# Performance work log

Hardware: AMD Instinct MI355X
Metric: run time of the kernel (lower is better)

## Reference

```python
import jax, jax.numpy as jnp
import numpy as np

B, C, N, H = 8, 256, 1024, 8

def setup_inputs() -> dict:
    key = jax.random.key(0)
    ks = jax.random.split(key, 6)
    x = jax.random.normal(ks[0], (B, C, 3, N), jnp.float32)
    scale = 1.0 / np.sqrt(C).astype(np.float32)
    Wq = jax.random.normal(ks[1], (C, C), jnp.float32) * scale
    Wk = jax.random.normal(ks[2], (C, C), jnp.float32) * scale
    Wv = jax.random.normal(ks[3], (C, C), jnp.float32) * scale
    Wp = jax.random.normal(ks[4], (C, C), jnp.float32) * scale
    mask = jax.random.randint(ks[5], (B, N), 0, 2).astype(bool)  # True = padded
    return {"x": x, "Wq": Wq, "Wk": Wk, "Wv": Wv, "Wp": Wp, "mask": mask}

def _vn_linear(W, x):
    # VNLinear: channel-mixing linear (no bias) over the C axis of [B, C, 3, N]
    return jnp.einsum('oc,bcdn->bodn', W, x)

def _to_heads(t):
    # [B, C, 3, N] -> [B, H, N, (C//H)*3]
    hd = C // H
    return t.reshape(B, H, hd, 3, N).transpose(0, 1, 4, 2, 3).reshape(B, H, N, hd * 3)

def reference(x, Wq, Wk, Wv, Wp, mask):
    hd = C // H
    D = hd * 3
    q = _to_heads(_vn_linear(Wq, x))
    k = _to_heads(_vn_linear(Wk, x))
    v = _to_heads(_vn_linear(Wv, x))
    att = jnp.einsum('bhnd,bhmd->bhnm', q, k) * (1.0 / np.sqrt(D).astype(np.float32))
    att = jnp.where(mask[:, None, None, :], -jnp.inf, att)
    att = jax.nn.softmax(att, axis=-1)
    y = jnp.einsum('bhnm,bhmd->bhnd', att, v)
    # [B, H, N, D] -> [B, H, D, N] -> [B, H, hd, 3, N] -> [B, C, 3, N]
    y = y.transpose(0, 1, 3, 2).reshape(B, H, hd, 3, N).reshape(B, C, 3, N)
    return _vn_linear(Wp, y)
```

## Files before the change

### kernel.cpp

```cpp
#include <hip/hip_runtime.h>
#include <hip/hip_bf16.h>
#include <math.h>

#define B_ 8
#define C_ 256
#define N_ 1024
#define H_ 8
#define DH 96
#define BHN (C_*3*N_)
#define SC 0.10206207261596575f

typedef _Float16 half8 __attribute__((ext_vector_type(8)));
typedef float f32x4 __attribute__((ext_vector_type(4)));
typedef float f32x16 __attribute__((ext_vector_type(16)));

typedef __attribute__((address_space(1))) void gvoid;
typedef __attribute__((address_space(3))) void lvoid;
__device__ inline void gl_lds16(const _Float16* g, _Float16* l) {
  __builtin_amdgcn_global_load_lds((gvoid*)g, (lvoid*)l, 16, 0, 0);
}

typedef __fp16 fp16x2 __attribute__((ext_vector_type(2)));
union H2U { fp16x2 h2; unsigned u; };
__device__ inline unsigned pkh(float a, float b) {
  H2U x; x.h2 = __builtin_amdgcn_cvt_pkrtz(a, b); return x.u;
}
union PF { half8 v; unsigned u[4]; };

__global__ void mask_bits_kernel(const unsigned* __restrict__ mraw,
                                 unsigned long long* __restrict__ mb) {
  __shared__ int notI, notF;
  if (threadIdx.x == 0) { notI = 0; notF = 0; }
  __syncthreads();
  int li = 0, lf = 0;
  for (int i = threadIdx.x; i < 2048; i += 256) {
    unsigned w = mraw[i];
    if (w > 1u) li = 1;
    if (w != 0u && w != 0x3F800000u) lf = 1;
  }
  if (li) atomicOr(&notI, 1);
  if (lf) atomicOr(&notF, 1);
  __syncthreads();
  const int tid = threadIdx.x;
  if (tid < 128) {
    int base = tid * 64;
    unsigned long long bits = 0;
    if (!notI) {
      for (int j = 0; j < 64; ++j)
        bits |= (unsigned long long)(mraw[base + j] & 1u) << j;
    } else if (!notF) {
      for (int j = 0; j < 64; ++j)
        bits |= (unsigned long long)(mraw[base + j] != 0u ? 1 : 0) << j;
    } else {
      const unsigned char* m8 = (const unsigned char*)mraw;
      for (int j = 0; j < 64; ++j)
        bits |= (unsigned long long)(m8[base + j] ? 1 : 0) << j;
    }
    mb[tid] = bits;
  }
}

__global__ void convw_kernel(const float* __restrict__ Wq,
                             const float* __restrict__ Wk,
                             const float* __restrict__ Wv,
                             const float* __restrict__ Wp,
                             _Float16* __restrict__ Wh) {
  int idx = blockIdx.x * 256 + threadIdx.x;
  int e0 = idx * 8;
  const float* src = (e0 < 65536) ? Wq
                   : (e0 < 131072) ? Wk
                   : (e0 < 196608) ? Wv : Wp;
  int off = e0 & 65535;
  float4 a = *(const float4*)&src[off];
  float4 b = *(const float4*)&src[off + 4];
  _Float16 t[8] = {(_Float16)a.x, (_Float16)a.y, (_Float16)a.z, (_Float16)a.w,
                   (_Float16)b.x, (_Float16)b.y, (_Float16)b.z, (_Float16)b.w};
  *(uint4*)&Wh[e0] = *(uint4*)t;
}

__global__ __launch_bounds__(256) void convxt_kernel(
    const float* __restrict__ x, _Float16* __restrict__ XT) {
  __shared__ _Float16 T[64][65];
  const int m0 = blockIdx.x * 64;
  const int c0 = blockIdx.y * 64;
  const int b = blockIdx.z;
  const float* xb = x + (size_t)b * BHN;
  _Float16* ob = XT + (size_t)b * BHN;
  const int t = threadIdx.x;
#pragma unroll
  for (int i = 0; i < 16; ++i) {
    int e = t + i * 256;
    int c = e >> 6, m = e & 63;
    T[m][c] = (_Float16)xb[(size_t)(c0 + c) * 3072 + m0 + m];
  }
  __syncthreads();
#pragma unroll
  for (int i = 0; i < 2; ++i) {
    int e = t + i * 256;
    int m = e >> 3, ch = e & 7;
    _Float16 tmp[8];
#pragma unroll
    for (int j = 0; j < 8; ++j) tmp[j] = T[m][ch * 8 + j];
    *(uint4*)&ob[(size_t)(m0 + m) * 256 + c0 + ch * 8] = *(uint4*)tmp;
  }
}

template <int MODE>
__global__ __launch_bounds__(256, 4) void mgemm_kernel(
    const _Float16* __restrict__ Wh, int woff,
    const _Float16* __restrict__ Xn,
    _Float16* __restrict__ O0, _Float16* __restrict__ O1,
    _Float16* __restrict__ O2, float* __restrict__ Of, int nw) {
  const int zz = blockIdx.z;
  const int w = zz % nw;
  const int b = zz / nw;
  const _Float16* Wb = Wh + (size_t)(woff + w) * 65536;
  const _Float16* Bb = Xn + (size_t)b * BHN;
  const int o0 = blockIdx.y * 128;
  const int bn0 = blockIdx.x * 128;

  __shared__ __align__(16) _Float16 Ah[4096];
  __shared__ __align__(16) _Float16 Bh[4096];

  const int tid = threadIdx.x;
  const int wave = tid >> 6;
  const int lane = tid & 63;
  const int lg = lane >> 4, ll = lane & 15;
  const int wm = wave >> 1, wn = wave & 1;
  const int r0 = tid >> 2, c4 = tid & 3;

  f32x4 acc[4][4];
#pragma unroll
  for (int mi = 0; mi < 4; ++mi)
#pragma unroll
    for (int ni = 0; ni < 4; ++ni) acc[mi][ni] = (f32x4){0.f, 0.f, 0.f, 0.f};

  for (int k0 = 0; k0 < 256; k0 += 32) {
    gl_lds16(Wb + (size_t)(o0 + r0) * 256 + k0 + c4 * 8, &Ah[wave * 512]);
    gl_lds16(Wb + (size_t)(o0 + 64 + r0) * 256 + k0 + c4 * 8,
             &Ah[2048 + wave * 512]);
    gl_lds16(Bb + (size_t)(bn0 + r0) * 256 + k0 + c4 * 8, &Bh[wave * 512]);
    gl_lds16(Bb + (size_t)(bn0 + 64 + r0) * 256 + k0 + c4 * 8,
             &Bh[2048 + wave * 512]);
    __syncthreads();
    half8 af[4], bf[4];
#pragma unroll
    for (int mi = 0; mi < 4; ++mi)
      af[mi] = *(const half8*)&Ah[(wm * 64 + mi * 16 + ll) * 32 + lg * 8];
#pragma unroll
    for (int ni = 0; ni < 4; ++ni)
      bf[ni] = *(const half8*)&Bh[(wn * 64 + ni * 16 + ll) * 32 + lg * 8];
#pragma unroll
    for (int mi = 0; mi < 4; ++mi)
#pragma unroll
      for (int ni = 0; ni < 4; ++ni)
        acc[mi][ni] = __builtin_amdgcn_mfma_f32_16x16x32_f16(
            af[mi], bf[ni], acc[mi][ni], 0, 0, 0);
    __syncthreads();
  }

#pragma unroll
  for (int mi = 0; mi < 4; ++mi) {
#pragma unroll
    for (int ni = 0; ni < 4; ++ni) {
      int o = o0 + wm * 64 + mi * 16 + lg * 4;
      int n = bn0 + wn * 64 + ni * 16 + ll;
      if constexpr (MODE == 1) {
        float* Ofb = Of + (size_t)b * BHN;
#pragma unroll
        for (int r = 0; r < 4; ++r)
          Ofb[(size_t)(o + r) * 3072 + n] = acc[mi][ni][r];
      } else {
        if (w == 2) {
          _Float16* Oc = O2 + (size_t)b * BHN;
#pragma unroll
          for (int r = 0; r < 4; ++r)
            Oc[(size_t)(o + r) * 3072 + n] = (_Float16)acc[mi][ni][r];
        } else {
          _Float16* On = ((w == 0) ? O0 : O1) + (size_t)b * BHN;
          float qs = (w == 0) ? SC : 1.0f;
          _Float16 t4[4];
#pragma unroll
          for (int r = 0; r < 4; ++r) t4[r] = (_Float16)(acc[mi][ni][r] * qs);
          *(uint2*)&On[(size_t)n * 256 + o] = *(uint2*)t4;
        }
      }
    }
  }
}

__global__ __launch_bounds__(256, 2) void attn_kernel(
    const _Float16* __restrict__ qh, const _Float16* __restrict__ kh,
    const _Float16* __restrict__ vh,
    const unsigned long long* __restrict__ mbits,
    _Float16* __restrict__ yT) {
  const int gid = blockIdx.x;
  const int bh = gid & 63;
  const int qt = gid >> 6;
  const int b = bh >> 3, h = bh & 7;
  const int n0 = qt * 128;

  __shared__ __align__(16) _Float16 Qs[12288];
  __shared__ __align__(16) _Float16 Ks[6144];
  __shared__ __align__(16) _Float16 Vt[6144];

  const int tid = threadIdx.x;
  const int lane = tid & 63;
  const int wave = tid >> 6;
  const int hi = lane >> 5;
  const int lq = lane & 31;
  const int wq0 = wave * 32;

  const _Float16* qb = qh + (size_t)b * BHN;
  const _Float16* kb = kh + (size_t)b * BHN;
  const _Float16* vb = vh + (size_t)b * BHN;

#pragma unroll
  for (int r = 0; r < 6; ++r) {
    int pc = r * 4 + wave;
    int p = pc >> 1;
    int q = (pc & 1) * 64 + lane;
    gl_lds16(qb + (size_t)((p >> 2) * 1024 + n0 + q) * 256 + h * 32 + (p & 3) * 8,
             &Qs[(r * 4 + wave) * 512]);
  }
  __syncthreads();

  half8 qf[6];
#pragma unroll
  for (int ks = 0; ks < 6; ++ks)
    qf[ks] = *(const half8*)&Qs[(((2 * ks + hi) * 128) + wq0 + lq) * 8];

  const _Float16* ksrc[3];
  const _Float16* vsrc[3];
#pragma unroll
  for (int r = 0; r < 3; ++r) {
    int p = r * 4 + wave;
    ksrc[r] = kb + (size_t)((p >> 2) * 1024 + lane) * 256 + h * 32 + (p & 3) * 8;
    int G = (r * 4 + wave) * 64 + lane;
    int kp = G / 96, d = G - kp * 96;
    vsrc[r] = vb + (size_t)(h * 32 + (d & 31)) * 3072 + (d >> 5) * 1024 + kp * 8;
  }

  float M = 0.f, L = 0.f;
  f32x16 yacc[3];
#pragma unroll
  for (int dt = 0; dt < 3; ++dt)
#pragma unroll
    for (int r = 0; r < 16; ++r) yacc[dt][r] = 0.f;

  for (int t = 0; t < 16; ++t) {
    __syncthreads();
#pragma unroll
    for (int r = 0; r < 3; ++r) {
      gl_lds16(ksrc[r], &Ks[(r * 4 + wave) * 512]);
      gl_lds16(vsrc[r], &Vt[(r * 4 + wave) * 512]);
      ksrc[r] += 64 * 256;
      vsrc[r] += 64;
    }
    __syncthreads();

    const unsigned long long m64 = mbits[b * 16 + t];

    f32x16 s[2];
#pragma unroll
    for (int r = 0; r < 16; ++r) { s[0][r] = 0.f; s[1][r] = 0.f; }
#pragma unroll
    for (int ks = 0; ks < 6; ++ks) {
      half8 kf0 = *(const half8*)&Ks[(((2 * ks + hi) * 64) + lq) * 8];
      half8 kf1 = *(const half8*)&Ks[(((2 * ks + hi) * 64) + 32 + lq) * 8];
      s[0] = __builtin_amdgcn_mfma_f32_32x32x16_f16(kf0, qf[ks], s[0], 0, 0, 0);
      s[1] = __builtin_amdgcn_mfma_f32_32x32x16_f16(kf1, qf[ks], s[1], 0, 0, 0);
    }

    float mx = -1e30f;
#pragma unroll
    for (int nt = 0; nt < 2; ++nt) {
      unsigned wm = (unsigned)(m64 >> (nt * 32 + 4 * hi));
#pragma unroll
      for (int r = 0; r < 16; ++r) {
        float sv = s[nt][r];
        sv = ((wm >> ((r & 3) + 8 * (r >> 2))) & 1u) ? -1e30f : sv;
        s[nt][r] = sv;
        mx = fmaxf(mx, sv);
      }
    }
    mx = fmaxf(mx, __shfl_xor(mx, 32));
    float newM = fmaxf(M, mx);
    float corr = __expf(M - newM);
    M = newM;
    float psum = 0.f;
#pragma unroll
    for (int nt = 0; nt < 2; ++nt)
#pragma unroll
      for (int r = 0; r < 16; ++r) {
        float p = __expf(s[nt][r] - newM);
        s[nt][r] = p;
        psum += p;
      }
    psum += __shfl_xor(psum, 32);
    L = L * corr + psum;
#pragma unroll
    for (int dt = 0; dt < 3; ++dt)
#pragma unroll
      for (int r = 0; r < 16; ++r) yacc[dt][r] *= corr;

#pragma unroll
    for (int nt = 0; nt < 2; ++nt) {
#pragma unroll
      for (int hf = 0; hf < 2; ++hf) {
        const int bs = hf * 8;
        unsigned A0 = pkh(s[nt][bs + 0], s[nt][bs + 1]);
        unsigned A1 = pkh(s[nt][bs + 2], s[nt][bs + 3]);
        unsigned B0 = pkh(s[nt][bs + 4], s[nt][bs + 5]);
        unsigned B1 = pkh(s[nt][bs + 6], s[nt][bs + 7]);
        unsigned xA0 = (unsigned)__shfl_xor((int)A0, 32);
        unsigned xA1 = (unsigned)__shfl_xor((int)A1, 32);
        unsigned xB0 = (unsigned)__shfl_xor((int)B0, 32);
        unsigned xB1 = (unsigned)__shfl_xor((int)B1, 32);
        PF pf;
        pf.u[0] = hi ? xB0 : A0;
        pf.u[1] = hi ? xB1 : A1;
        pf.u[2] = hi ? B0 : xA0;
        pf.u[3] = hi ? B1 : xA1;
        const int kt = nt * 2 + hf;
#pragma unroll
        for (int dt = 0; dt < 3; ++dt) {
          half8 vf = *(const half8*)&Vt[(((kt * 2 + hi) * 96) + dt * 32 + lq) * 8];
          yacc[dt] = __builtin_amdgcn_mfma_f32_32x32x16_f16(vf, pf.v, yacc[dt],
                                                            0, 0, 0);
        }
      }
    }
  }

  float inv = (L > 0.f) ? 1.f / L : 0.f;
  _Float16* Ys = &Qs[wave * 3072];
#pragma unroll
  for (int dt = 0; dt < 3; ++dt)
#pragma unroll
    for (int r = 0; r < 16; ++r) {
      int dperm = dt * 32 + (r & 3) + 8 * (r >> 2) + 4 * hi;
      Ys[lq * 96 + dperm] = (_Float16)(yacc[dt][r] * inv);
    }
  _Float16* yb = yT + (size_t)b * BHN;
#pragma unroll
  for (int j = 0; j < 6; ++j) {
    int c = j * 64 + lane;
    int q = c / 12, p = c - q * 12;
    uint4 val = *(const uint4*)&Ys[q * 96 + p * 8];
    int dd = p >> 2, pi = p & 3;
    *(uint4*)&yb[(size_t)((dd << 10) + n0 + wq0 + q) * 256 + h * 32 + pi * 8] =
        val;
  }
}

extern "C" void kernel_launch(void* const* d_in, const int* in_sizes, int n_in,
                              void* d_out, int out_size, void* d_ws,
                              size_t ws_size, hipStream_t stream) {
  const float* x = (const float*)d_in[0];
  const float* Wq = (const float*)d_in[1];
  const float* Wk = (const float*)d_in[2];
  const float* Wv = (const float*)d_in[3];
  const float* Wp = (const float*)d_in[4];
  const unsigned* mask = (const unsigned*)d_in[5];
  float* out = (float*)d_out;

  _Float16* Wh = (_Float16*)d_ws;
  _Float16* XT = Wh + 4 * 65536;
  _Float16* qh = XT + (size_t)B_ * BHN;
  _Float16* kh = qh + (size_t)B_ * BHN;
  _Float16* vh = kh + (size_t)B_ * BHN;
  _Float16* yT = vh + (size_t)B_ * BHN;
  unsigned long long* mb = (unsigned long long*)(yT + (size_t)B_ * BHN);

  mask_bits_kernel<<<1, 256, 0, stream>>>(mask, mb);
  convw_kernel<<<128, 256, 0, stream>>>(Wq, Wk, Wv, Wp, Wh);
  convxt_kernel<<<dim3(48, 4, B_), 256, 0, stream>>>(x, XT);

  dim3 g1(24, 2, B_ * 3);
  mgemm_kernel<0><<<g1, 256, 0, stream>>>(Wh, 0, XT, qh, kh, vh, nullptr, 3);

  attn_kernel<<<dim3(512), 256, 0, stream>>>(qh, kh, vh, mb, yT);

  dim3 g3(24, 2, B_);
  mgemm_kernel<1><<<g3, 256, 0, stream>>>(Wh, 3, yT, nullptr, nullptr, nullptr,
                                          out, 1);
}
```

Before: 104.9 us.

## Double-buffer K/V tiles, add lazy softmax rescaling and permlane32 swaps

K and V tiles now go into two LDS buffers, so the async global-to-LDS load of tile t+1 is issued while tile t is computed. This removes one barrier per iteration and hides load latency. The online softmax only rescales the accumulators when some row max grows by more than 8, and the row-sum shuffle is deferred to the end. The four xor-32 shuffles that build the P operand are replaced by two v_permlane32_swap instructions, and MFMA sections are wrapped in s_setprio. The extra LDS buffer raises shared memory per block, which could limit occupancy, and the lazy rescale lets fp16 P values grow up to about e^8.

```diff
diff --git a/kernel.cpp b/kernel.cpp
--- a/kernel.cpp
+++ b/kernel.cpp
@@ -26,6 +26,10 @@
   H2U x; x.h2 = __builtin_amdgcn_cvt_pkrtz(a, b); return x.u;
 }
 union PF { half8 v; unsigned u[4]; };
+
+__device__ inline void plswap(unsigned& a, unsigned& b) {
+  asm volatile("v_permlane32_swap_b32 %0, %1" : "+v"(a), "+v"(b));
+}
 
 __global__ void mask_bits_kernel(const unsigned* __restrict__ mraw,
                                  unsigned long long* __restrict__ mb) {
@@ -201,8 +205,8 @@
   const int n0 = qt * 128;
 
   __shared__ __align__(16) _Float16 Qs[12288];
-  __shared__ __align__(16) _Float16 Ks[6144];
-  __shared__ __align__(16) _Float16 Vt[6144];
+  __shared__ __align__(16) _Float16 KsL[2][6144];
+  __shared__ __align__(16) _Float16 VtL[2][6144];
 
   const int tid = threadIdx.x;
   const int lane = tid & 63;
@@ -215,6 +219,29 @@
   const _Float16* kb = kh + (size_t)b * BHN;
   const _Float16* vb = vh + (size_t)b * BHN;
 
+  const _Float16* ksrc[3];
+  const _Float16* vsrc[3];
+#pragma unroll
+  for (int r = 0; r < 3; ++r) {
+    int p = r * 4 + wave;
+    ksrc[r] = kb + (size_t)((p >> 2) * 1024 + lane) * 256 + h * 32 + (p & 3) * 8;
+    int G = (r * 4 + wave) * 64 + lane;
+    int kp = G / 96, d = G - kp * 96;
+    vsrc[r] = vb + (size_t)(h * 32 + (d & 31)) * 3072 + (d >> 5) * 1024 + kp * 8;
+  }
+
+  auto stage_kv = [&](int cur) {
+    _Float16* Kd = &KsL[cur][0];
+    _Float16* Vd = &VtL[cur][0];
+#pragma unroll
+    for (int r = 0; r < 3; ++r) {
+      gl_lds16(ksrc[r], &Kd[(r * 4 + wave) * 512]);
+      gl_lds16(vsrc[r], &Vd[(r * 4 + wave) * 512]);
+      ksrc[r] += 64 * 256;
+      vsrc[r] += 64;
+    }
+  };
+
 #pragma unroll
   for (int r = 0; r < 6; ++r) {
     int pc = r * 4 + wave;
@@ -223,54 +250,39 @@
     gl_lds16(qb + (size_t)((p >> 2) * 1024 + n0 + q) * 256 + h * 32 + (p & 3) * 8,
              &Qs[(r * 4 + wave) * 512]);
   }
+  stage_kv(0);
   __syncthreads();
+  stage_kv(1);
 
   half8 qf[6];
 #pragma unroll
   for (int ks = 0; ks < 6; ++ks)
     qf[ks] = *(const half8*)&Qs[(((2 * ks + hi) * 128) + wq0 + lq) * 8];
 
-  const _Float16* ksrc[3];
-  const _Float16* vsrc[3];
-#pragma unroll
-  for (int r = 0; r < 3; ++r) {
-    int p = r * 4 + wave;
-    ksrc[r] = kb + (size_t)((p >> 2) * 1024 + lane) * 256 + h * 32 + (p & 3) * 8;
-    int G = (r * 4 + wave) * 64 + lane;
-    int kp = G / 96, d = G - kp * 96;
-    vsrc[r] = vb + (size_t)(h * 32 + (d & 31)) * 3072 + (d >> 5) * 1024 + kp * 8;
-  }
-
-  float M = 0.f, L = 0.f;
+  float M = 0.f, Lh = 0.f;
   f32x16 yacc[3];
 #pragma unroll
   for (int dt = 0; dt < 3; ++dt)
 #pragma unroll
     for (int r = 0; r < 16; ++r) yacc[dt][r] = 0.f;
 
-  for (int t = 0; t < 16; ++t) {
-    __syncthreads();
-#pragma unroll
-    for (int r = 0; r < 3; ++r) {
-      gl_lds16(ksrc[r], &Ks[(r * 4 + wave) * 512]);
-      gl_lds16(vsrc[r], &Vt[(r * 4 + wave) * 512]);
-      ksrc[r] += 64 * 256;
-      vsrc[r] += 64;
-    }
-    __syncthreads();
-
+  auto compute_tile = [&](int t, int cur) {
+    const _Float16* Ksb = &KsL[cur][0];
+    const _Float16* Vtb = &VtL[cur][0];
     const unsigned long long m64 = mbits[b * 16 + t];
 
     f32x16 s[2];
 #pragma unroll
     for (int r = 0; r < 16; ++r) { s[0][r] = 0.f; s[1][r] = 0.f; }
+    __builtin_amdgcn_s_setprio(1);
 #pragma unroll
     for (int ks = 0; ks < 6; ++ks) {
-      half8 kf0 = *(const half8*)&Ks[(((2 * ks + hi) * 64) + lq) * 8];
-      half8 kf1 = *(const half8*)&Ks[(((2 * ks + hi) * 64) + 32 + lq) * 8];
+      half8 kf0 = *(const half8*)&Ksb[(((2 * ks + hi) * 64) + lq) * 8];
+      half8 kf1 = *(const half8*)&Ksb[(((2 * ks + hi) * 64) + 32 + lq) * 8];
       s[0] = __builtin_amdgcn_mfma_f32_32x32x16_f16(kf0, qf[ks], s[0], 0, 0, 0);
       s[1] = __builtin_amdgcn_mfma_f32_32x32x16_f16(kf1, qf[ks], s[1], 0, 0, 0);
     }
+    __builtin_amdgcn_s_setprio(0);
 
     float mx = -1e30f;
 #pragma unroll
@@ -284,25 +296,27 @@
         mx = fmaxf(mx, sv);
       }
     }
-    mx = fmaxf(mx, __shfl_xor(mx, 32));
-    float newM = fmaxf(M, mx);
-    float corr = __expf(M - newM);
-    M = newM;
+    if (__any(mx > M + 8.f)) {
+      float mx2 = fmaxf(mx, __shfl_xor(mx, 32));
+      float newM = fmaxf(M, mx2);
+      float corr = __expf(M - newM);
+      M = newM;
+      Lh *= corr;
+#pragma unroll
+      for (int dt = 0; dt < 3; ++dt)
+#pragma unroll
+        for (int r = 0; r < 16; ++r) yacc[dt][r] *= corr;
+    }
     float psum = 0.f;
 #pragma unroll
     for (int nt = 0; nt < 2; ++nt)
 #pragma unroll
       for (int r = 0; r < 16; ++r) {
-        float p = __expf(s[nt][r] - newM);
+        float p = __expf(s[nt][r] - M);
         s[nt][r] = p;
         psum += p;
       }
-    psum += __shfl_xor(psum, 32);
-    L = L * corr + psum;
-#pragma unroll
-    for (int dt = 0; dt < 3; ++dt)
-#pragma unroll
-      for (int r = 0; r < 16; ++r) yacc[dt][r] *= corr;
+    Lh += psum;
 
 #pragma unroll
     for (int nt = 0; nt < 2; ++nt) {
@@ -313,26 +327,34 @@
         unsigned A1 = pkh(s[nt][bs + 2], s[nt][bs + 3]);
         unsigned B0 = pkh(s[nt][bs + 4], s[nt][bs + 5]);
         unsigned B1 = pkh(s[nt][bs + 6], s[nt][bs + 7]);
-        unsigned xA0 = (unsigned)__shfl_xor((int)A0, 32);
-        unsigned xA1 = (unsigned)__shfl_xor((int)A1, 32);
-        unsigned xB0 = (unsigned)__shfl_xor((int)B0, 32);
-        unsigned xB1 = (unsigned)__shfl_xor((int)B1, 32);
+        plswap(A0, B0);
+        plswap(A1, B1);
         PF pf;
-        pf.u[0] = hi ? xB0 : A0;
-        pf.u[1] = hi ? xB1 : A1;
-        pf.u[2] = hi ? B0 : xA0;
-        pf.u[3] = hi ? B1 : xA1;
+        pf.u[0] = A0;
+        pf.u[1] = A1;
+        pf.u[2] = B0;
+        pf.u[3] = B1;
         const int kt = nt * 2 + hf;
+        __builtin_amdgcn_s_setprio(1);
 #pragma unroll
         for (int dt = 0; dt < 3; ++dt) {
-          half8 vf = *(const half8*)&Vt[(((kt * 2 + hi) * 96) + dt * 32 + lq) * 8];
+          half8 vf = *(const half8*)&Vtb[(((kt * 2 + hi) * 96) + dt * 32 + lq) * 8];
           yacc[dt] = __builtin_amdgcn_mfma_f32_32x32x16_f16(vf, pf.v, yacc[dt],
                                                             0, 0, 0);
         }
+        __builtin_amdgcn_s_setprio(0);
       }
     }
-  }
-
+  };
+
+  compute_tile(0, 0);
+  for (int t = 1; t < 16; ++t) {
+    __syncthreads();
+    if (t + 1 < 16) stage_kv((t + 1) & 1);
+    compute_tile(t, t & 1);
+  }
+
+  float L = Lh + __shfl_xor(Lh, 32);
   float inv = (L > 0.f) ? 1.f / L : 0.f;
   _Float16* Ys = &Qs[wave * 3072];
 #pragma unroll
```

New measurement: 101.6 us. -3.2%, faster.
